# Kernel optimization log

Hardware: AMD Instinct MI355X
Metric: run time of the kernel (lower is better)

Reference implementation:

```python
import jax, jax.numpy as jnp
import numpy as np

H = 2048          # hidden size
N_HEADS = 16
HEAD_DIM = H // N_HEADS   # 128
ATTN_SCALE = 8.0          # attention_scale > 1.0 -> custom max-subtract path
B, S = 2, 2048


def setup_inputs() -> dict:
    key = jax.random.key(0)
    k1, k2, k3, k4, k5 = jax.random.split(key, 5)
    hidden_states = jax.random.normal(k1, (B, S, H), dtype=jnp.float32)
    # causal left-to-right multiplicative mask, broadcast over batch and heads
    ltor_mask = jnp.tril(jnp.ones((S, S), dtype=jnp.float32))[None, None]
    std = 0.02
    W_qkv = jax.random.normal(k2, (H, 3 * H), dtype=jnp.float32) * std
    b_qkv = jnp.zeros((3 * H,), dtype=jnp.float32)
    W_out = jax.random.normal(k3, (H, H), dtype=jnp.float32) * std
    b_out = jnp.zeros((H,), dtype=jnp.float32)
    return {"hidden_states": hidden_states, "ltor_mask": ltor_mask,
            "W_qkv": W_qkv, "b_qkv": b_qkv, "W_out": W_out, "b_out": b_out}


def reference(hidden_states, ltor_mask, W_qkv, b_qkv, W_out, b_out):
    b, s, h = hidden_states.shape
    # fused QKV projection: [b, s, 3h]
    qkv = jnp.einsum('bsh,hk->bsk', hidden_states, W_qkv) + b_qkv
    q, k, v = jnp.split(qkv, 3, axis=-1)
    # [b, s, h] -> [b, n, s, hn]
    def to_heads(t):
        return t.reshape(b, s, N_HEADS, HEAD_DIM).transpose(0, 2, 1, 3)
    q, k, v = to_heads(q), to_heads(k), to_heads(v)
    # custom scale: q / sqrt(scale), k / sqrt(hn * scale)
    inv = 1.0 / (ATTN_SCALE * np.sqrt(np.float32(HEAD_DIM)))
    scores = jnp.einsum('bnqd,bnkd->bnqk', q, k) * jnp.float32(inv)
    # multiplicative mask BEFORE max-subtract (zeroes masked positions)
    scores = scores * ltor_mask
    # attention_scale > 1.0 path: subtract row max, re-multiply by scale
    scores = (scores - jnp.max(scores, axis=-1, keepdims=True)) * jnp.float32(ATTN_SCALE)
    # additive large-negative fill on masked entries
    scores = scores + jnp.float32(-65504.0) * (1.0 - ltor_mask)
    probs = jax.nn.softmax(scores, axis=-1)
    ctx = jnp.einsum('bnqk,bnkd->bnqd', probs, v)
    ctx = ctx.transpose(0, 2, 1, 3).reshape(b, s, h)
    out = jnp.einsum('bsh,hk->bsk', ctx, W_out) + b_out
    return out
```

## Files before the change

kernel.cpp:

```cpp
#include <hip/hip_runtime.h>

#define S_LEN 2048
#define HDIM  2048
#define NHEADS 16
#define DHEAD 128
#define BATCH 2
#define MROWS (BATCH * S_LEN)
#define QKVN  (3 * HDIM)

typedef _Float16 f16;
typedef _Float16 f16x8 __attribute__((ext_vector_type(8)));
typedef _Float16 f16x4 __attribute__((ext_vector_type(4)));
typedef float    f32x4 __attribute__((ext_vector_type(4)));
typedef float    f32x16 __attribute__((ext_vector_type(16)));

typedef const __attribute__((address_space(1))) void* gas_ptr;
typedef __attribute__((address_space(3))) void*       las_ptr;

#define MFMA16(a, b, c)  __builtin_amdgcn_mfma_f32_16x16x32_f16(a, b, c, 0, 0, 0)
#define MFMA32(a, b, c)  __builtin_amdgcn_mfma_f32_32x32x16_f16(a, b, c, 0, 0, 0)

__device__ __forceinline__ void gl_lds16(const f16* g, f16* lds_wave_base) {
  __builtin_amdgcn_global_load_lds((gas_ptr)g, (las_ptr)lds_wave_base, 16, 0, 0);
}


__device__ __forceinline__ void transpose_tile(const float* __restrict__ W,
                                               f16* __restrict__ Wb,
                                               int K, int N, int k0, int n0,
                                               float* tile ) {
  int tr = threadIdx.x >> 4;
  int tc = (threadIdx.x & 15) * 4;
  int KT = K >> 5;
#pragma unroll
  for (int rr = 0; rr < 4; ++rr) {
    int r = rr * 16 + tr;
    float4 v = *(const float4*)(W + (size_t)(k0 + r) * N + n0 + tc);
    tile[r * 65 + tc + 0] = v.x; tile[r * 65 + tc + 1] = v.y;
    tile[r * 65 + tc + 2] = v.z; tile[r * 65 + tc + 3] = v.w;
  }
  __syncthreads();
#pragma unroll
  for (int rr = 0; rr < 4; ++rr) {
    int r = rr * 16 + tr;
    int n = n0 + r;
    int kBase = k0 + tc;
    f16x4 o;
#pragma unroll
    for (int c = 0; c < 4; ++c) o[c] = (f16)tile[(tc + c) * 65 + r];
    int nt = n >> 7, nn = n & 127;
    int kt = kBase >> 5, kc = (kBase >> 3) & 3, j = kBase & 7;
    *(f16x4*)(Wb + ((size_t)nt * KT + kt) * 4096 + (kc * 128 + nn) * 8 + j) = o;
  }
}

__global__ __launch_bounds__(256) void prep_kernel(const float* __restrict__ X,
                                                   f16* __restrict__ Xb,
                                                   const float* __restrict__ Wqkv,
                                                   f16* __restrict__ Wqkvb,
                                                   const float* __restrict__ Wout,
                                                   f16* __restrict__ Woutb) {
  __shared__ float tile[64 * 65];
  int bz = blockIdx.x;
  if (bz < 2048) {
    int kt = bz & 63, rt = bz >> 6;
    int t = threadIdx.x;
    int m = t >> 1, half = t & 1;
    const float* src = X + (size_t)(rt * 128 + m) * HDIM + kt * 32 + half * 16;
    float4 v0 = ((const float4*)src)[0];
    float4 v1 = ((const float4*)src)[1];
    float4 v2 = ((const float4*)src)[2];
    float4 v3 = ((const float4*)src)[3];
    f16x8 a = {(f16)v0.x, (f16)v0.y, (f16)v0.z, (f16)v0.w,
               (f16)v1.x, (f16)v1.y, (f16)v1.z, (f16)v1.w};
    f16x8 b = {(f16)v2.x, (f16)v2.y, (f16)v2.z, (f16)v2.w,
               (f16)v3.x, (f16)v3.y, (f16)v3.z, (f16)v3.w};
    f16* dst = Xb + ((size_t)rt * 64 + kt) * 4096 + ((half * 2) * 128 + m) * 8;
    *(f16x8*)dst = a;
    *(f16x8*)(dst + 1024) = b;
  } else if (bz < 5120) {
    int u = bz - 2048;
    int nx = u % 96, ky = u / 96;
    transpose_tile(Wqkv, Wqkvb, HDIM, QKVN, ky * 64, nx * 64, tile);
  } else {
    int u = bz - 5120;
    int nx = u & 31, ky = u >> 5;
    transpose_tile(Wout, Woutb, HDIM, HDIM, ky * 64, nx * 64, tile);
  }
}

template <int MODE>
__global__ __launch_bounds__(512, 2) void gemm256_kernel(const f16* __restrict__ Ablk,
                                                         const f16* __restrict__ Bblk,
                                                         const float* __restrict__ bias,
                                                         f16* __restrict__ Cpart,
                                                         f16* __restrict__ Qr,
                                                         f16* __restrict__ KB,
                                                         f16* __restrict__ VB,
                                                         int M, int N, int K) {
  __shared__ f16 As[4][2][4096];
  __shared__ f16 Bs[4][2][4096];
  const int tid = threadIdx.x;
  const int lane = tid & 63, wv = tid >> 6;
  const int lhi = lane >> 4, llo = lane & 15;
  const int wr = wv >> 2, wc = wv & 3;
  const int bx = blockIdx.x, by = blockIdx.y;
  const int KT = K >> 5;
  int t0 = 0, ntiles = KT;
  if (MODE == 2) { ntiles = KT >> 1; t0 = blockIdx.z * ntiles; }

  const f16* Ab0 = Ablk + ((size_t)(2 * by)     * KT + t0) * 4096;
  const f16* Ab1 = Ablk + ((size_t)(2 * by + 1) * KT + t0) * 4096;
  const f16* Bb0 = Bblk + ((size_t)(2 * bx)     * KT + t0) * 4096;
  const f16* Bb1 = Bblk + ((size_t)(2 * bx + 1) * KT + t0) * 4096;

  f32x4 acc[8][4];
#pragma unroll
  for (int i = 0; i < 8; ++i)
#pragma unroll
    for (int j = 0; j < 4; ++j) acc[i][j] = (f32x4){0.f, 0.f, 0.f, 0.f};

  auto stA = [&](int bufi, int kt) {
    gl_lds16(Ab0 + (size_t)kt * 4096 + tid * 8, &As[bufi][0][0] + wv * 512);
    gl_lds16(Ab1 + (size_t)kt * 4096 + tid * 8, &As[bufi][1][0] + wv * 512);
  };
  auto stB = [&](int bufi, int kt) {
    gl_lds16(Bb0 + (size_t)kt * 4096 + tid * 8, &Bs[bufi][0][0] + wv * 512);
    gl_lds16(Bb1 + (size_t)kt * 4096 + tid * 8, &Bs[bufi][1][0] + wv * 512);
  };

#pragma unroll
  for (int u = 0; u < 3; ++u) { stA(u, u); stB(u, u); }

  for (int t = 0; t < ntiles; ++t) {
    const int buf = t & 3;
    const bool st = (t + 3 < ntiles);
    const int nb = (t + 3) & 3, ntile = t + 3;

    if (t + 2 < ntiles)      asm volatile("s_waitcnt vmcnt(8)" ::: "memory");
    else if (t + 1 < ntiles) asm volatile("s_waitcnt vmcnt(4)" ::: "memory");
    else                     asm volatile("s_waitcnt vmcnt(0)" ::: "memory");
    __builtin_amdgcn_s_barrier();

    const f16* Ah = &As[buf][wr][0];
    const f16* Bh = &Bs[buf][wc >> 1][0];
    f16x8 bfr[4], afr[4];

#pragma unroll
    for (int j = 0; j < 4; ++j)
      bfr[j] = *(const f16x8*)(Bh + (lhi * 128 + (wc & 1) * 64 + j * 16 + llo) * 8);
#pragma unroll
    for (int i = 0; i < 4; ++i)
      afr[i] = *(const f16x8*)(Ah + (lhi * 128 + i * 16 + llo) * 8);
    if (st) stA(nb, ntile);
    __builtin_amdgcn_s_barrier();
    asm volatile("s_waitcnt lgkmcnt(0)" ::: "memory");
    __builtin_amdgcn_s_setprio(1);
#pragma unroll
    for (int i = 0; i < 4; ++i)
#pragma unroll
      for (int j = 0; j < 4; ++j) acc[i][j] = MFMA16(afr[i], bfr[j], acc[i][j]);
    __builtin_amdgcn_s_setprio(0);
    __builtin_amdgcn_s_barrier();

#pragma unroll
    for (int i = 0; i < 4; ++i)
      afr[i] = *(const f16x8*)(Ah + (lhi * 128 + (i + 4) * 16 + llo) * 8);
    if (st) stB(nb, ntile);
    __builtin_amdgcn_s_barrier();
    asm volatile("s_waitcnt lgkmcnt(0)" ::: "memory");
    __builtin_amdgcn_s_setprio(1);
#pragma unroll
    for (int i = 0; i < 4; ++i)
#pragma unroll
      for (int j = 0; j < 4; ++j) acc[i + 4][j] = MFMA16(afr[i], bfr[j], acc[i + 4][j]);
    __builtin_amdgcn_s_setprio(0);
  }

#pragma unroll
  for (int j = 0; j < 4; ++j) {
    int col = bx * 256 + wc * 64 + j * 16 + llo;
    float bv = (MODE == 1) ? bias[col] : 0.f;
#pragma unroll
    for (int i = 0; i < 8; ++i) {
      int rowb = by * 256 + wr * 128 + i * 16 + lhi * 4;
      if (MODE == 2) {
        size_t zoff = (size_t)blockIdx.z * M * N;
#pragma unroll
        for (int r = 0; r < 4; ++r)
          Cpart[zoff + (size_t)(rowb + r) * N + col] = (f16)acc[i][j][r];
      } else {
        int region = col >> 11;
        if (region == 0) {
#pragma unroll
          for (int r = 0; r < 4; ++r)
            Qr[(size_t)(rowb + r) * HDIM + col] = (f16)(acc[i][j][r] + bv);
        } else if (region == 1) {
          int cK = col - HDIM;
          int hd = cK >> 7, d = cK & 127, g = d >> 3, dj = d & 7;
#pragma unroll
          for (int r = 0; r < 4; ++r) {
            int row = rowb + r;
            int b = row >> 11, s = row & 2047;
            int kt2 = s >> 6, key = s & 63;
            size_t addr = ((((size_t)(b * 16 + hd) * 32 + kt2) * 16 + g) * 64 + key) * 8 + dj;
            KB[addr] = (f16)(acc[i][j][r] + bv);
          }
        } else {
          int cV = col - 2 * HDIM;
          int hd = cV >> 7, d = cV & 127;
          int row = rowb;
          int b = row >> 11, s = row & 2047;
          int kt2 = s >> 6, key = s & 63;
          int kg = key >> 3, kj = key & 7;
          f16x4 pv = {(f16)(acc[i][j][0] + bv), (f16)(acc[i][j][1] + bv),
                      (f16)(acc[i][j][2] + bv), (f16)(acc[i][j][3] + bv)};
          size_t addr = ((((size_t)(b * 16 + hd) * 32 + kt2) * 8 + kg) * 128 + d) * 8 + kj;
          *(f16x4*)(VB + addr) = pv;
        }
      }
    }
  }
}

__global__ __launch_bounds__(256) void merge_out_kernel(const f16* __restrict__ Cpart,
                                                        const float* __restrict__ bias,
                                                        float* __restrict__ out) {
  int t = blockIdx.x * 256 + threadIdx.x;
  int col8 = (t & 255) * 8;
  int row = t >> 8;
  size_t base = (size_t)row * HDIM + col8;
  const size_t MN = (size_t)MROWS * HDIM;
  f16x8 a = *(const f16x8*)(Cpart + base);
  f16x8 b = *(const f16x8*)(Cpart + MN + base);
  float4 b0 = *(const float4*)(bias + col8);
  float4 b1 = *(const float4*)(bias + col8 + 4);
  float4 o0 = {(float)a[0] + (float)b[0] + b0.x, (float)a[1] + (float)b[1] + b0.y,
               (float)a[2] + (float)b[2] + b0.z, (float)a[3] + (float)b[3] + b0.w};
  float4 o1 = {(float)a[4] + (float)b[4] + b1.x, (float)a[5] + (float)b[5] + b1.y,
               (float)a[6] + (float)b[6] + b1.z, (float)a[7] + (float)b[7] + b1.w};
  *(float4*)(out + base) = o0;
  *(float4*)(out + base + 4) = o1;
}

__global__ __launch_bounds__(256, 3) void attn_kernel(const f16* __restrict__ Qr,
                                                      const f16* __restrict__ KB,
                                                      const f16* __restrict__ VB,
                                                      f16* __restrict__ Opart,
                                                      float* __restrict__ Lpart) {
  __shared__ f16 Ks[1024 * 8];
  __shared__ f16 Vs[1024 * 8];
  __shared__ f16 Ps[4][32 * 72];

  int tid = threadIdx.x, lane = tid & 63, w = tid >> 6;
  int l5 = lane & 31, hl = lane >> 5;
  int bh = blockIdx.y, b = bh >> 4, hd = bh & 15;
  int gx = blockIdx.x;
  int qt, kt0, kt1, slot;
  if (gx < 8) { qt = gx; slot = 0; kt0 = 0; kt1 = 2 * qt + 2; }
  else {
    qt = 8 + ((gx - 8) >> 1); slot = (gx - 8) & 1;
    kt0 = slot ? (qt + 1) : 0;
    kt1 = slot ? (2 * qt + 2) : (qt + 1);
  }

  int qbase = qt * 128 + w * 32;
  int qrow = qbase + l5;

  const f16* qp = Qr + (size_t)(b * S_LEN + qrow) * HDIM + hd * DHEAD + hl * 8;
  f16x8 qf[8];
#pragma unroll
  for (int s8 = 0; s8 < 8; ++s8) qf[s8] = *(const f16x8*)(qp + s8 * 16);

  f32x16 oac[4];
#pragma unroll
  for (int mt = 0; mt < 4; ++mt)
#pragma unroll
    for (int r = 0; r < 16; ++r) oac[mt][r] = 0.f;
  float rs = 0.f;

  const float C1 = 0.12752747419986393f;
  const float C2 = 11.541560327111708f;

  const f16* KBb = KB + (size_t)bh * 32 * 8192;
  const f16* VBb = VB + (size_t)bh * 32 * 8192;

  for (int kt = kt0; kt < kt1; ++kt) {
    __syncthreads();
    {
      const f16* Kt = KBb + (size_t)kt * 8192;
      const f16* Vt = VBb + (size_t)kt * 8192;
#pragma unroll
      for (int c = 0; c < 4; ++c) {
        int u0 = w * 256 + c * 64;
        gl_lds16(Kt + (size_t)(u0 + lane) * 8, Ks + u0 * 8);
        gl_lds16(Vt + (size_t)(u0 + lane) * 8, Vs + u0 * 8);
      }
    }
    __syncthreads();

    if (kt * 64 <= qbase + 31) {
      f32x16 sac[2];
#pragma unroll
      for (int mt = 0; mt < 2; ++mt)
#pragma unroll
        for (int r = 0; r < 16; ++r) sac[mt][r] = 0.f;
#pragma unroll
      for (int s8 = 0; s8 < 8; ++s8) {
#pragma unroll
        for (int mt = 0; mt < 2; ++mt) {
          f16x8 kf = *(const f16x8*)(Ks + ((s8 * 2 + hl) * 64 + mt * 32 + l5) * 8);
          sac[mt] = MFMA32(kf, qf[s8], sac[mt]);
        }
      }

      bool diag = (kt * 64 + 63 > qbase);
#pragma unroll
      for (int mt = 0; mt < 2; ++mt) {
#pragma unroll
        for (int g4 = 0; g4 < 4; ++g4) {
          f16x4 pk;
#pragma unroll
          for (int r = 0; r < 4; ++r) {
            int keyl = mt * 32 + g4 * 8 + hl * 4 + r;
            float p = __builtin_amdgcn_exp2f(fmaf(sac[mt][g4 * 4 + r], C1, -C2));
            if (diag && (kt * 64 + keyl > qrow)) p = 0.f;
            rs += p;
            pk[r] = (f16)p;
          }
          *(f16x4*)(&Ps[w][l5 * 72 + mt * 32 + g4 * 8 + hl * 4]) = pk;
        }
      }
      asm volatile("s_waitcnt lgkmcnt(0)" ::: "memory");

#pragma unroll
      for (int ks = 0; ks < 4; ++ks) {
        f16x8 pf = *(const f16x8*)(&Ps[w][l5 * 72 + ks * 16 + hl * 8]);
#pragma unroll
        for (int mt = 0; mt < 4; ++mt) {
          f16x8 vf = *(const f16x8*)(Vs + ((ks * 2 + hl) * 128 + mt * 32 + l5) * 8);
          oac[mt] = MFMA32(vf, pf, oac[mt]);
        }
      }
    }
  }

  float lsum = rs + __shfl_xor(rs, 32, 64);
  size_t ob = ((size_t)slot * 32 + bh) * S_LEN * DHEAD + (size_t)qrow * DHEAD;
#pragma unroll
  for (int mt = 0; mt < 4; ++mt) {
#pragma unroll
    for (int g4 = 0; g4 < 4; ++g4) {
      int d = mt * 32 + g4 * 8 + hl * 4;
      f16x4 ov = {(f16)oac[mt][g4 * 4 + 0], (f16)oac[mt][g4 * 4 + 1],
                  (f16)oac[mt][g4 * 4 + 2], (f16)oac[mt][g4 * 4 + 3]};
      *(f16x4*)(Opart + ob + d) = ov;
    }
  }
  if (hl == 0) Lpart[((size_t)slot * 32 + bh) * S_LEN + qrow] = lsum;
}

__global__ __launch_bounds__(256) void merge_kernel(const f16* __restrict__ Opart,
                                                    const float* __restrict__ Lpart,
                                                    f16* __restrict__ CTXb) {
  int t = blockIdx.x * 256 + threadIdx.x;
  int d8 = (t & 15) * 8;
  int q = (t >> 4) & 2047;
  int bh = t >> 15;
  int b = bh >> 4, hd = bh & 15;
  int ns = ((q >> 7) >= 8) ? 2 : 1;
  size_t o0 = ((size_t)bh * S_LEN + q) * DHEAD + d8;
  const size_t OSLOT = (size_t)32 * S_LEN * DHEAD;
  float l = Lpart[(size_t)bh * S_LEN + q];
  f16x8 a = *(const f16x8*)(Opart + o0);
  float acc[8];
#pragma unroll
  for (int j = 0; j < 8; ++j) acc[j] = (float)a[j];
  if (ns == 2) {
    l += Lpart[OSLOT / DHEAD + (size_t)bh * S_LEN + q];
    f16x8 a2 = *(const f16x8*)(Opart + OSLOT + o0);
#pragma unroll
    for (int j = 0; j < 8; ++j) acc[j] += (float)a2[j];
  }
  float inv = 1.0f / l;
  f16x8 o;
#pragma unroll
  for (int j = 0; j < 8; ++j) o[j] = (f16)(acc[j] * inv);
  int row = b * S_LEN + q;
  int col = hd * DHEAD + d8;
  int rt = row >> 7, rr = row & 127;
  int kt = col >> 5, kc = (col >> 3) & 3;
  *(f16x8*)(CTXb + ((size_t)rt * 64 + kt) * 4096 + (kc * 128 + rr) * 8) = o;
}

extern "C" void kernel_launch(void* const* d_in, const int* in_sizes, int n_in,
                              void* d_out, int out_size, void* d_ws, size_t ws_size,
                              hipStream_t stream) {
  const float* X    = (const float*)d_in[0];
  const float* Wqkv = (const float*)d_in[2];
  const float* bqkv = (const float*)d_in[3];
  const float* Wout = (const float*)d_in[4];
  const float* bout = (const float*)d_in[5];
  float* out = (float*)d_out;

  char* ws = (char*)d_ws;
  f16* Xb    = (f16*)ws;  ws += (size_t)MROWS * HDIM * sizeof(f16);
  f16* Wqkvb = (f16*)ws;  ws += (size_t)QKVN * HDIM * sizeof(f16);
  f16* Woutb = (f16*)ws;  ws += (size_t)HDIM * HDIM * sizeof(f16);
  f16* Qr    = (f16*)ws;  ws += (size_t)MROWS * HDIM * sizeof(f16);
  f16* KB    = (f16*)ws;  ws += (size_t)32 * 32 * 8192 * sizeof(f16);
  f16* VB    = (f16*)ws;  ws += (size_t)32 * 32 * 8192 * sizeof(f16);
  f16* Opart = (f16*)ws;  ws += (size_t)2 * 32 * S_LEN * DHEAD * sizeof(f16);
  float* Lpart = (float*)ws;  ws += (size_t)2 * 32 * S_LEN * sizeof(float);
  f16* CTXb  = Xb;
  f16* Cpart = Opart;

  prep_kernel<<<6144, 256, 0, stream>>>(X, Xb, Wqkv, Wqkvb, Wout, Woutb);

  gemm256_kernel<1><<<dim3(QKVN / 256, MROWS / 256), 512, 0, stream>>>(
      Xb, Wqkvb, bqkv, nullptr, Qr, KB, VB, MROWS, QKVN, HDIM);

  attn_kernel<<<dim3(24, 32), 256, 0, stream>>>(Qr, KB, VB, Opart, Lpart);

  merge_kernel<<<(32 * S_LEN * 16) / 256, 256, 0, stream>>>(Opart, Lpart, CTXb);

  gemm256_kernel<2><<<dim3(HDIM / 256, MROWS / 256, 2), 512, 0, stream>>>(
      CTXb, Woutb, nullptr, Cpart, nullptr, nullptr, nullptr, MROWS, HDIM, HDIM);

  merge_out_kernel<<<(MROWS * HDIM / 8) / 256, 256, 0, stream>>>(Cpart, bout, out);
}
```

Measured before the change: 406.8 us.

## Remap block indices per XCD and merge GEMM LDS fragment loads per k-tile

Block IDs in both GEMM modes and in the attention kernel are remapped so that blocks landing on the same XCD (hardware assigns blocks round-robin across 8 XCDs) share A/B row panels or attention heads. The intent is better L2 reuse. The GEMM inner loop now loads both halves of the A fragments up front and issues both async global-to-LDS stores, dropping two barriers and the lgkmcnt waits between the MFMA halves. This adds register pressure with the extra afr2 array. It also risks races: the next tile is written into buffer nb while other waves may still be reading, and LDS reads are not explicitly waited before the MFMAs.

```diff
diff --git a/kernel.cpp b/kernel.cpp
--- a/kernel.cpp
+++ b/kernel.cpp
@@ -104,10 +104,24 @@
   const int lane = tid & 63, wv = tid >> 6;
   const int lhi = lane >> 4, llo = lane & 15;
   const int wr = wv >> 2, wc = wv & 3;
-  const int bx = blockIdx.x, by = blockIdx.y;
+
+  int bx, by, bz = 0;
+  if (MODE == 1) {
+    int lin = blockIdx.x + 24 * blockIdx.y;
+    int xcd = lin & 7, slot = lin >> 3;
+    bx = (xcd >> 1) * 6 + slot % 6;
+    by = (xcd & 1) * 8 + slot / 6;
+  } else {
+    int lin = blockIdx.x + 8 * (blockIdx.y + 16 * blockIdx.z);
+    int xcd = lin & 7, slot = lin >> 3;
+    bx = slot & 7;
+    by = (xcd >> 1) * 4 + (slot >> 3);
+    bz = xcd & 1;
+  }
+
   const int KT = K >> 5;
   int t0 = 0, ntiles = KT;
-  if (MODE == 2) { ntiles = KT >> 1; t0 = blockIdx.z * ntiles; }
+  if (MODE == 2) { ntiles = KT >> 1; t0 = bz * ntiles; }
 
   const f16* Ab0 = Ablk + ((size_t)(2 * by)     * KT + t0) * 4096;
   const f16* Ab1 = Ablk + ((size_t)(2 * by + 1) * KT + t0) * 4096;
@@ -144,7 +158,7 @@
 
     const f16* Ah = &As[buf][wr][0];
     const f16* Bh = &Bs[buf][wc >> 1][0];
-    f16x8 bfr[4], afr[4];
+    f16x8 bfr[4], afr[4], afr2[4];
 
 #pragma unroll
     for (int j = 0; j < 4; ++j)
@@ -153,27 +167,20 @@
     for (int i = 0; i < 4; ++i)
       afr[i] = *(const f16x8*)(Ah + (lhi * 128 + i * 16 + llo) * 8);
     if (st) stA(nb, ntile);
-    __builtin_amdgcn_s_barrier();
-    asm volatile("s_waitcnt lgkmcnt(0)" ::: "memory");
+#pragma unroll
+    for (int i = 0; i < 4; ++i)
+      afr2[i] = *(const f16x8*)(Ah + (lhi * 128 + (i + 4) * 16 + llo) * 8);
+    if (st) stB(nb, ntile);
+
     __builtin_amdgcn_s_setprio(1);
 #pragma unroll
     for (int i = 0; i < 4; ++i)
 #pragma unroll
       for (int j = 0; j < 4; ++j) acc[i][j] = MFMA16(afr[i], bfr[j], acc[i][j]);
-    __builtin_amdgcn_s_setprio(0);
-    __builtin_amdgcn_s_barrier();
-
 #pragma unroll
     for (int i = 0; i < 4; ++i)
-      afr[i] = *(const f16x8*)(Ah + (lhi * 128 + (i + 4) * 16 + llo) * 8);
-    if (st) stB(nb, ntile);
-    __builtin_amdgcn_s_barrier();
-    asm volatile("s_waitcnt lgkmcnt(0)" ::: "memory");
-    __builtin_amdgcn_s_setprio(1);
-#pragma unroll
-    for (int i = 0; i < 4; ++i)
-#pragma unroll
-      for (int j = 0; j < 4; ++j) acc[i + 4][j] = MFMA16(afr[i], bfr[j], acc[i + 4][j]);
+#pragma unroll
+      for (int j = 0; j < 4; ++j) acc[i + 4][j] = MFMA16(afr2[i], bfr[j], acc[i + 4][j]);
     __builtin_amdgcn_s_setprio(0);
   }
 
@@ -185,7 +192,7 @@
     for (int i = 0; i < 8; ++i) {
       int rowb = by * 256 + wr * 128 + i * 16 + lhi * 4;
       if (MODE == 2) {
-        size_t zoff = (size_t)blockIdx.z * M * N;
+        size_t zoff = (size_t)bz * M * N;
 #pragma unroll
         for (int r = 0; r < 4; ++r)
           Cpart[zoff + (size_t)(rowb + r) * N + col] = (f16)acc[i][j][r];
@@ -254,8 +261,13 @@
 
   int tid = threadIdx.x, lane = tid & 63, w = tid >> 6;
   int l5 = lane & 31, hl = lane >> 5;
-  int bh = blockIdx.y, b = bh >> 4, hd = bh & 15;
-  int gx = blockIdx.x;
+
+  int lin0 = blockIdx.x + 24 * blockIdx.y;
+  int xcd0 = lin0 & 7, slot0 = lin0 >> 3;
+  int bh = xcd0 * 4 + slot0 / 24;
+  int gx = slot0 % 24;
+
+  int b = bh >> 4, hd = bh & 15;
   int qt, kt0, kt1, slot;
   if (gx < 8) { qt = gx; slot = 0; kt0 = 0; kt1 = 2 * qt + 2; }
   else {
```

Result: no change. 411.9 us (+1.3%).

## Use 256x384 QKV GEMM tiles and XCD-aware block remapping across kernels

Applied to the files above, without the earlier changes.

The QKV projection gets its own kernel with a 256x384 output tile, triple-buffered LDS and three staged MFMA phases per k-step. The grid then shrinks to 256 blocks, one wave of work across the CUs, which removes the partial tail wave of the previous 384-block launch. Block indices in the QKV GEMM, the output GEMM and the attention kernel are remapped so that blocks sharing A/B tiles or heads land on the same XCD, for better L2 reuse. The price is more accumulator registers (48 f32x4) and a shallower prefetch pipeline, which may cause spills or weaker latency hiding.

```diff
diff --git a/kernel.cpp b/kernel.cpp
--- a/kernel.cpp
+++ b/kernel.cpp
@@ -89,25 +89,160 @@
   }
 }
 
-template <int MODE>
-__global__ __launch_bounds__(512, 2) void gemm256_kernel(const f16* __restrict__ Ablk,
-                                                         const f16* __restrict__ Bblk,
-                                                         const float* __restrict__ bias,
-                                                         f16* __restrict__ Cpart,
-                                                         f16* __restrict__ Qr,
-                                                         f16* __restrict__ KB,
-                                                         f16* __restrict__ VB,
-                                                         int M, int N, int K) {
+__global__ __launch_bounds__(512, 2) void gemm_qkv_kernel(const f16* __restrict__ Ablk,
+                                                          const f16* __restrict__ Bblk,
+                                                          const float* __restrict__ bias,
+                                                          f16* __restrict__ Qr,
+                                                          f16* __restrict__ KB,
+                                                          f16* __restrict__ VB) {
+  __shared__ f16 As[3][2][4096];
+  __shared__ f16 Bs[3][3][4096];
+  const int tid = threadIdx.x;
+  const int lane = tid & 63, wv = tid >> 6;
+  const int lhi = lane >> 4, llo = lane & 15;
+  const int wr = wv >> 2, wc = wv & 3;
+
+  int lin = blockIdx.x + 16 * blockIdx.y;
+  int xcd = lin & 7, slot = lin >> 3;
+  int bx = (xcd & 3) * 4 + (slot & 3);
+  int by = (xcd >> 2) * 8 + (slot >> 2);
+
+  const int KT = HDIM >> 5;
+  const f16* Ab0 = Ablk + (size_t)(2 * by)     * KT * 4096;
+  const f16* Ab1 = Ablk + (size_t)(2 * by + 1) * KT * 4096;
+  const f16* Bb0 = Bblk + (size_t)(3 * bx)     * KT * 4096;
+  const f16* Bb1 = Bblk + (size_t)(3 * bx + 1) * KT * 4096;
+  const f16* Bb2 = Bblk + (size_t)(3 * bx + 2) * KT * 4096;
+
+  f32x4 acc[8][6];
+#pragma unroll
+  for (int i = 0; i < 8; ++i)
+#pragma unroll
+    for (int j = 0; j < 6; ++j) acc[i][j] = (f32x4){0.f, 0.f, 0.f, 0.f};
+
+  auto stA = [&](int bufi, int kt) {
+    gl_lds16(Ab0 + (size_t)kt * 4096 + tid * 8, &As[bufi][0][0] + wv * 512);
+    gl_lds16(Ab1 + (size_t)kt * 4096 + tid * 8, &As[bufi][1][0] + wv * 512);
+  };
+  auto stB = [&](int bufi, int kt) {
+    gl_lds16(Bb0 + (size_t)kt * 4096 + tid * 8, &Bs[bufi][0][0] + wv * 512);
+    gl_lds16(Bb1 + (size_t)kt * 4096 + tid * 8, &Bs[bufi][1][0] + wv * 512);
+    gl_lds16(Bb2 + (size_t)kt * 4096 + tid * 8, &Bs[bufi][2][0] + wv * 512);
+  };
+  auto rdB = [&](int bufi, int j) -> f16x8 {
+    int cg = wc * 96 + j * 16;
+    return *(const f16x8*)(&Bs[bufi][cg >> 7][0] + (lhi * 128 + (cg & 127) + llo) * 8);
+  };
+
+  stA(0, 0); stB(0, 0);
+  stA(1, 1); stB(1, 1);
+
+  for (int t = 0; t < KT; ++t) {
+    const int buf = t % 3;
+    const bool st = (t + 2 < KT);
+    const int nb = (t + 2) % 3;
+
+    if (t + 1 < KT) asm volatile("s_waitcnt vmcnt(5)" ::: "memory");
+    else            asm volatile("s_waitcnt vmcnt(0)" ::: "memory");
+    __builtin_amdgcn_s_barrier();
+
+    const f16* Ah = &As[buf][wr][0];
+    f16x8 afr[8], bA, bB;
+
+#pragma unroll
+    for (int i = 0; i < 8; ++i)
+      afr[i] = *(const f16x8*)(Ah + (lhi * 128 + i * 16 + llo) * 8);
+    bA = rdB(buf, 0); bB = rdB(buf, 1);
+    if (st) stA(nb, t + 2);
+    __builtin_amdgcn_s_barrier();
+    asm volatile("s_waitcnt lgkmcnt(0)" ::: "memory");
+    __builtin_amdgcn_s_setprio(1);
+#pragma unroll
+    for (int i = 0; i < 8; ++i) acc[i][0] = MFMA16(afr[i], bA, acc[i][0]);
+#pragma unroll
+    for (int i = 0; i < 8; ++i) acc[i][1] = MFMA16(afr[i], bB, acc[i][1]);
+    __builtin_amdgcn_s_setprio(0);
+
+    bA = rdB(buf, 2); bB = rdB(buf, 3);
+    if (st) stB(nb, t + 2);
+    __builtin_amdgcn_s_barrier();
+    asm volatile("s_waitcnt lgkmcnt(0)" ::: "memory");
+    __builtin_amdgcn_s_setprio(1);
+#pragma unroll
+    for (int i = 0; i < 8; ++i) acc[i][2] = MFMA16(afr[i], bA, acc[i][2]);
+#pragma unroll
+    for (int i = 0; i < 8; ++i) acc[i][3] = MFMA16(afr[i], bB, acc[i][3]);
+    __builtin_amdgcn_s_setprio(0);
+
+    bA = rdB(buf, 4); bB = rdB(buf, 5);
+    __builtin_amdgcn_s_barrier();
+    asm volatile("s_waitcnt lgkmcnt(0)" ::: "memory");
+    __builtin_amdgcn_s_setprio(1);
+#pragma unroll
+    for (int i = 0; i < 8; ++i) acc[i][4] = MFMA16(afr[i], bA, acc[i][4]);
+#pragma unroll
+    for (int i = 0; i < 8; ++i) acc[i][5] = MFMA16(afr[i], bB, acc[i][5]);
+    __builtin_amdgcn_s_setprio(0);
+  }
+
+#pragma unroll
+  for (int j = 0; j < 6; ++j) {
+    int col = bx * 384 + wc * 96 + j * 16 + llo;
+    float bv = bias[col];
+#pragma unroll
+    for (int i = 0; i < 8; ++i) {
+      int rowb = by * 256 + wr * 128 + i * 16 + lhi * 4;
+      int region = col >> 11;
+      if (region == 0) {
+#pragma unroll
+        for (int r = 0; r < 4; ++r)
+          Qr[(size_t)(rowb + r) * HDIM + col] = (f16)(acc[i][j][r] + bv);
+      } else if (region == 1) {
+        int cK = col - HDIM;
+        int hd = cK >> 7, d = cK & 127, g = d >> 3, dj = d & 7;
+#pragma unroll
+        for (int r = 0; r < 4; ++r) {
+          int row = rowb + r;
+          int b = row >> 11, s = row & 2047;
+          int kt2 = s >> 6, key = s & 63;
+          size_t addr = ((((size_t)(b * 16 + hd) * 32 + kt2) * 16 + g) * 64 + key) * 8 + dj;
+          KB[addr] = (f16)(acc[i][j][r] + bv);
+        }
+      } else {
+        int cV = col - 2 * HDIM;
+        int hd = cV >> 7, d = cV & 127;
+        int row = rowb;
+        int b = row >> 11, s = row & 2047;
+        int kt2 = s >> 6, key = s & 63;
+        int kg = key >> 3, kj = key & 7;
+        f16x4 pv = {(f16)(acc[i][j][0] + bv), (f16)(acc[i][j][1] + bv),
+                    (f16)(acc[i][j][2] + bv), (f16)(acc[i][j][3] + bv)};
+        size_t addr = ((((size_t)(b * 16 + hd) * 32 + kt2) * 8 + kg) * 128 + d) * 8 + kj;
+        *(f16x4*)(VB + addr) = pv;
+      }
+    }
+  }
+}
+
+__global__ __launch_bounds__(512, 2) void gemm_out_kernel(const f16* __restrict__ Ablk,
+                                                          const f16* __restrict__ Bblk,
+                                                          f16* __restrict__ Cpart) {
   __shared__ f16 As[4][2][4096];
   __shared__ f16 Bs[4][2][4096];
   const int tid = threadIdx.x;
   const int lane = tid & 63, wv = tid >> 6;
   const int lhi = lane >> 4, llo = lane & 15;
   const int wr = wv >> 2, wc = wv & 3;
-  const int bx = blockIdx.x, by = blockIdx.y;
-  const int KT = K >> 5;
-  int t0 = 0, ntiles = KT;
-  if (MODE == 2) { ntiles = KT >> 1; t0 = blockIdx.z * ntiles; }
+
+  int lin = blockIdx.x + 8 * (blockIdx.y + 16 * blockIdx.z);
+  int xcd = lin & 7, slot = lin >> 3;
+  int bx = slot & 7;
+  int by = (xcd >> 1) * 4 + (slot >> 3);
+  int bz = xcd & 1;
+
+  const int KT = HDIM >> 5;
+  const int ntiles = KT >> 1;
+  const int t0 = bz * ntiles;
 
   const f16* Ab0 = Ablk + ((size_t)(2 * by)     * KT + t0) * 4096;
   const f16* Ab1 = Ablk + ((size_t)(2 * by + 1) * KT + t0) * 4096;
@@ -180,45 +315,13 @@
 #pragma unroll
   for (int j = 0; j < 4; ++j) {
     int col = bx * 256 + wc * 64 + j * 16 + llo;
-    float bv = (MODE == 1) ? bias[col] : 0.f;
 #pragma unroll
     for (int i = 0; i < 8; ++i) {
       int rowb = by * 256 + wr * 128 + i * 16 + lhi * 4;
-      if (MODE == 2) {
-        size_t zoff = (size_t)blockIdx.z * M * N;
-#pragma unroll
-        for (int r = 0; r < 4; ++r)
-          Cpart[zoff + (size_t)(rowb + r) * N + col] = (f16)acc[i][j][r];
-      } else {
-        int region = col >> 11;
-        if (region == 0) {
-#pragma unroll
-          for (int r = 0; r < 4; ++r)
-            Qr[(size_t)(rowb + r) * HDIM + col] = (f16)(acc[i][j][r] + bv);
-        } else if (region == 1) {
-          int cK = col - HDIM;
-          int hd = cK >> 7, d = cK & 127, g = d >> 3, dj = d & 7;
-#pragma unroll
-          for (int r = 0; r < 4; ++r) {
-            int row = rowb + r;
-            int b = row >> 11, s = row & 2047;
-            int kt2 = s >> 6, key = s & 63;
-            size_t addr = ((((size_t)(b * 16 + hd) * 32 + kt2) * 16 + g) * 64 + key) * 8 + dj;
-            KB[addr] = (f16)(acc[i][j][r] + bv);
-          }
-        } else {
-          int cV = col - 2 * HDIM;
-          int hd = cV >> 7, d = cV & 127;
-          int row = rowb;
-          int b = row >> 11, s = row & 2047;
-          int kt2 = s >> 6, key = s & 63;
-          int kg = key >> 3, kj = key & 7;
-          f16x4 pv = {(f16)(acc[i][j][0] + bv), (f16)(acc[i][j][1] + bv),
-                      (f16)(acc[i][j][2] + bv), (f16)(acc[i][j][3] + bv)};
-          size_t addr = ((((size_t)(b * 16 + hd) * 32 + kt2) * 8 + kg) * 128 + d) * 8 + kj;
-          *(f16x4*)(VB + addr) = pv;
-        }
-      }
+      size_t zoff = (size_t)bz * MROWS * HDIM;
+#pragma unroll
+      for (int r = 0; r < 4; ++r)
+        Cpart[zoff + (size_t)(rowb + r) * HDIM + col] = (f16)acc[i][j][r];
     }
   }
 }
@@ -254,8 +357,13 @@
 
   int tid = threadIdx.x, lane = tid & 63, w = tid >> 6;
   int l5 = lane & 31, hl = lane >> 5;
-  int bh = blockIdx.y, b = bh >> 4, hd = bh & 15;
-  int gx = blockIdx.x;
+
+  int lin0 = blockIdx.x + 24 * blockIdx.y;
+  int xcd0 = lin0 & 7, slot0 = lin0 >> 3;
+  int bh = xcd0 * 4 + slot0 / 24;
+  int gx = slot0 % 24;
+
+  int b = bh >> 4, hd = bh & 15;
   int qt, kt0, kt1, slot;
   if (gx < 8) { qt = gx; slot = 0; kt0 = 0; kt1 = 2 * qt + 2; }
   else {
@@ -417,15 +525,15 @@
 
   prep_kernel<<<6144, 256, 0, stream>>>(X, Xb, Wqkv, Wqkvb, Wout, Woutb);
 
-  gemm256_kernel<1><<<dim3(QKVN / 256, MROWS / 256), 512, 0, stream>>>(
-      Xb, Wqkvb, bqkv, nullptr, Qr, KB, VB, MROWS, QKVN, HDIM);
+  gemm_qkv_kernel<<<dim3(QKVN / 384, MROWS / 256), 512, 0, stream>>>(
+      Xb, Wqkvb, bqkv, Qr, KB, VB);
 
   attn_kernel<<<dim3(24, 32), 256, 0, stream>>>(Qr, KB, VB, Opart, Lpart);
 
   merge_kernel<<<(32 * S_LEN * 16) / 256, 256, 0, stream>>>(Opart, Lpart, CTXb);
 
-  gemm256_kernel<2><<<dim3(HDIM / 256, MROWS / 256, 2), 512, 0, stream>>>(
-      CTXb, Woutb, nullptr, Cpart, nullptr, nullptr, nullptr, MROWS, HDIM, HDIM);
+  gemm_out_kernel<<<dim3(HDIM / 256, MROWS / 256, 2), 512, 0, stream>>>(
+      CTXb, Woutb, Cpart);
 
   merge_out_kernel<<<(MROWS * HDIM / 8) / 256, 256, 0, stream>>>(Cpart, bout, out);
 }
```

After: 375.2 us. 7.8% less time.
